# Kernel tuning notes

Measured on AMD Instinct MI355X. Metric: run time of the kernel, lower is better.

The kernel has to match this reference:

```python
import jax, jax.numpy as jnp
import numpy as np

B, S, H = 2, 1024, 2048
NH, NKV, HD = 32, 8, 64          # head_dim = H // NH
G = NH // NKV                    # GQA group size = 4
THETA = 500000.0
EPS = 1e-5
SCALE = HD ** -0.5


def _rope_neox(x, positions):
    # x: [B, S, n_heads, HD]; neox style: rotate concatenated halves
    inv_freq = 1.0 / (THETA ** (jnp.arange(0, HD, 2, dtype=jnp.float32) / HD))  # [HD/2]
    ang = positions[..., None].astype(jnp.float32) * inv_freq                    # [B, S, HD/2]
    cos = jnp.cos(ang)[:, :, None, :]
    sin = jnp.sin(ang)[:, :, None, :]
    x1, x2 = jnp.split(x, 2, axis=-1)
    return jnp.concatenate([x1 * cos - x2 * sin, x2 * cos + x1 * sin], axis=-1)


def setup_inputs() -> dict:
    key = jax.random.key(0)
    k1, k2, k3 = jax.random.split(key, 3)
    hidden_states = jax.random.normal(k1, (B, S, H), jnp.float32)
    w_qkv = jax.random.normal(k2, ((NH + 2 * NKV) * HD, H), jnp.float32) * 0.02
    w_o = jax.random.normal(k3, (H, NH * HD), jnp.float32) * 0.02
    norm_w = jnp.ones((H,), jnp.float32)
    positions = jnp.broadcast_to(jnp.arange(S, dtype=jnp.int32), (B, S))
    return {"hidden_states": hidden_states, "positions": positions,
            "w_qkv": w_qkv, "w_o": w_o, "norm_w": norm_w}


def reference(hidden_states, positions, w_qkv, w_o, norm_w):
    # QKV projection (bias=False) and split
    qkv = hidden_states @ w_qkv.T                                 # [B,S,3072]
    q, k, v = jnp.split(qkv, [NH * HD, NH * HD + NKV * HD], axis=-1)
    q = q.reshape(B, S, NH, HD)
    k = k.reshape(B, S, NKV, HD)
    v = v.reshape(B, S, NKV, HD)

    # RoPE on q and k (full rotary_dim = head_dim)
    q = _rope_neox(q, positions)
    k = _rope_neox(k, positions)

    # Causal GQA attention (dense-prefill equivalent of RadixAttention)
    qg = q.reshape(B, S, NKV, G, HD)
    scores = jnp.einsum('bqhgd,bkhd->bhgqk', qg, k) * SCALE       # [B,NKV,G,S,S]
    causal = jnp.tril(jnp.ones((S, S), dtype=bool))
    scores = jnp.where(causal, scores, jnp.float32(-1e30))
    probs = jax.nn.softmax(scores, axis=-1)
    attn = jnp.einsum('bhgqk,bkhd->bqhgd', probs, v).reshape(B, S, NH * HD)

    # BitNet sub-norm (RMSNorm) then output projection
    var = jnp.mean(attn * attn, axis=-1, keepdims=True)
    normed = attn * jax.lax.rsqrt(var + EPS) * norm_w
    return normed @ w_o.T                                         # [B,S,H]
```

## Files before the change

kernel.cpp:

```cpp
#include <hip/hip_runtime.h>
#include <hip/hip_bf16.h>
#include <cstdint>
#include <cstddef>

typedef __bf16 bf16;
typedef __bf16 bf16x2 __attribute__((ext_vector_type(2)));
typedef __bf16 bf16x4 __attribute__((ext_vector_type(4)));
typedef __bf16 bf16x8 __attribute__((ext_vector_type(8)));
typedef float  f32x4  __attribute__((ext_vector_type(4)));

__device__ __forceinline__ void async_copy16(const void* g, void* l) {
  __builtin_amdgcn_global_load_lds((const __attribute__((address_space(1))) void*)g,
                                   (__attribute__((address_space(3))) void*)l,
                                   16, 0, 0);
}

__device__ __forceinline__ int swz(int row) { return ((row >> 1) & 3) << 3; }

__device__ __forceinline__ bool block_flag_is_f32(const unsigned int* w, int tid,
                                                  int* sflag) {
  if (tid < 64) {
    int weird = 0;
#pragma unroll
    for (int c = 0; c < 2; ++c) {
      const unsigned int lo = w[c * 64 + tid] & 0xffffu;
      const unsigned int ex = (lo >> 7) & 0xffu;
      if (ex >= 134u) ++weird;
    }
    const unsigned long long m1 = __ballot(weird >= 1);
    const unsigned long long m2 = __ballot(weird == 2);
    if (tid == 0) *sflag = (__popcll(m1) + __popcll(m2) >= 8) ? 1 : 0;
  }
  __syncthreads();
  return *sflag != 0;
}

__global__ __launch_bounds__(256) void convert_all(
    const void* __restrict__ s0, const void* __restrict__ s1,
    const void* __restrict__ s2, const void* __restrict__ s3,
    bf16* __restrict__ d0, bf16* __restrict__ d1, bf16* __restrict__ d2,
    float* __restrict__ ssum) {
  __shared__ int sflag;
  const int tid = threadIdx.x;
  const bool f32 = block_flag_is_f32((const unsigned int*)s0, tid, &sflag);
  if (blockIdx.x == 0) {
    ((float4*)ssum)[tid * 2]     = make_float4(0.f, 0.f, 0.f, 0.f);
    ((float4*)ssum)[tid * 2 + 1] = make_float4(0.f, 0.f, 0.f, 0.f);
  }
  const int i = blockIdx.x * 256 + tid;
  if (i >= 3670016) return;
  const void* src; bf16* dst; int off; bool fold = false;
  if      (i < 1048576) { src = s0; dst = d0; off = i; }
  else if (i < 2621440) { src = s1; dst = d1; off = i - 1048576; }
  else                  { src = s2; dst = d2; off = i - 2621440; fold = true; }
  float v[4];
  if (f32) {
    const float4 t = ((const float4*)src)[off];
    v[0] = t.x; v[1] = t.y; v[2] = t.z; v[3] = t.w;
  } else {
    const bf16x4 t = ((const bf16x4*)src)[off];
#pragma unroll
    for (int j = 0; j < 4; ++j) v[j] = (float)t[j];
  }
  if (fold) {
    const int k0 = (off * 4) & 2047;
#pragma unroll
    for (int j = 0; j < 4; ++j) {
      const float w = f32 ? ((const float*)s3)[k0 + j] : (float)((const bf16*)s3)[k0 + j];
      v[j] *= w;
    }
  }
  bf16x4 o;
#pragma unroll
  for (int j = 0; j < 4; ++j) o[j] = (bf16)v[j];
  *(bf16x4*)(dst + (size_t)off * 4) = o;
}

__global__ __launch_bounds__(256) void gemm_qkv_rope(
    const bf16* __restrict__ A, const bf16* __restrict__ B,
    const int* __restrict__ pos,
    bf16* __restrict__ Q, bf16* __restrict__ K, bf16* __restrict__ V)
{
  __shared__ __align__(16) bf16 As[2][2 * 64 * 32];
  __shared__ __align__(16) bf16 Bs[2][2 * 128 * 32];
  const int tid = threadIdx.x, wave = tid >> 6, lane = tid & 63;
  const int l15 = lane & 15, l4 = lane >> 4;
  const int m0 = blockIdx.y * 64, n0 = blockIdx.x * 128;
  const int wm = (wave >> 1) * 32, wn = (wave & 1) * 64;
  const int swz_ro = (l4 * 8) ^ swz(l15);

  f32x4 acc[2][4] = {};

  auto stage = [&](int buf, int kt) {
#pragma unroll
    for (int c = 0; c < 2; ++c) {
      const int e = c * 2048 + tid * 8;
      const int kc = e >> 11, row = (e >> 5) & 63;
      const int o = (e & 31) ^ swz(row);
      async_copy16(A + (size_t)(m0 + row) * 2048 + kt + kc * 32 + o, &As[buf][e]);
    }
#pragma unroll
    for (int c = 0; c < 4; ++c) {
      const int e = c * 2048 + tid * 8;
      const int kc = e >> 12, row = (e >> 5) & 127;
      const int o = (e & 31) ^ swz(row);
      async_copy16(B + (size_t)(n0 + row) * 2048 + kt + kc * 32 + o, &Bs[buf][e]);
    }
  };

  stage(0, 0);
  __syncthreads();
  int cur = 0;
  for (int kt = 0; kt < 2048; kt += 64) {
    if (kt + 64 < 2048) stage(cur ^ 1, kt + 64);
#pragma unroll
    for (int s = 0; s < 2; ++s) {
      bf16x8 af[2], bfr[4];
#pragma unroll
      for (int i = 0; i < 2; ++i)
        af[i] = *(const bf16x8*)(&As[cur][s * 2048 + (wm + i * 16 + l15) * 32 + swz_ro]);
#pragma unroll
      for (int j = 0; j < 4; ++j)
        bfr[j] = *(const bf16x8*)(&Bs[cur][s * 4096 + (wn + j * 16 + l15) * 32 + swz_ro]);
#pragma unroll
      for (int i = 0; i < 2; ++i)
#pragma unroll
        for (int j = 0; j < 4; ++j)
          acc[i][j] = __builtin_amdgcn_mfma_f32_16x16x32_bf16(af[i], bfr[j], acc[i][j], 0, 0, 0);
    }
    __syncthreads();
    cur ^= 1;
  }

  if (n0 < 2560) {
    const bool isQ = (n0 < 2048);
#pragma unroll
    for (int i = 0; i < 2; ++i)
#pragma unroll
      for (int j = 0; j < 4; ++j) {
        const int col = n0 + wn + j * 16 + l15;
        const int hd = isQ ? col : (col - 2048);
        const int hh = hd >> 6, d = hd & 63;
        const int fi = d & 31;
        const float ifr = __expf((float)fi * -0.41007385554f);
#pragma unroll
        for (int r = 0; r < 4; ++r) {
          const int m = m0 + wm + i * 16 + l4 * 4 + r;
          const int b = m >> 10, s = m & 1023;
          const float ang = (float)pos[m] * ifr;
          float sn, cs;
          __sincosf(ang, &sn, &cs);
          const float x  = acc[i][j][r];
          const float xp = acc[i][j ^ 2][r];
          const float v = (d < 32) ? (x * cs - xp * sn) : (x * cs + xp * sn);
          if (isQ) Q[(((size_t)(b * 32 + hh)) * 1024 + s) * 64 + d] = (bf16)(v * 0.1803368801f);
          else     K[(((size_t)(b * 8 + hh)) * 1024 + s) * 64 + d] = (bf16)v;
        }
      }
  } else {
#pragma unroll
    for (int i = 0; i < 2; ++i)
#pragma unroll
      for (int j = 0; j < 4; ++j) {
        const int cv = n0 + wn + j * 16 + l15 - 2560;
        const int hh = cv >> 6, d = cv & 63;
#pragma unroll
        for (int r = 0; r < 4; ++r) {
          const int m = m0 + wm + i * 16 + l4 * 4 + r;
          const int b = m >> 10, s = m & 1023;
          const int sp = (s & ~31) + ((s & 15) * 2 + ((s >> 4) & 1));
          V[(((size_t)(b * 8 + hh)) * 64 + d) * 1024 + sp] = (bf16)acc[i][j][r];
        }
      }
  }
}

__global__ __launch_bounds__(256) void attn_kernel(
    const bf16* __restrict__ Q, const bf16* __restrict__ K,
    const bf16* __restrict__ Vt, bf16* __restrict__ O, float* __restrict__ ssum)
{
  __shared__ __align__(16) bf16 Ks[2 * 128 * 32];
  __shared__ __align__(16) bf16 Vs[4 * 64 * 32];
  __shared__ __align__(16) bf16 Ps[4 * 128 * 40];

  const int tid = threadIdx.x, wave = tid >> 6, lane = tid & 63;
  const int l15 = lane & 15, l4 = lane >> 4;
  const int swz_ro = (l4 * 8) ^ swz(l15);
  const int ip = blockIdx.x, bh = blockIdx.y;
  const int b = bh >> 5, h = bh & 31, kvh = h >> 2;
  const int qlo = ip * 64, qhi = (15 - ip) * 64;
  const bf16* Qb = Q + ((size_t)(b * 32 + h)) * 65536;
  const bf16* Kb = K + ((size_t)(b * 8 + kvh)) * 65536;
  const bf16* Vb = Vt + ((size_t)(b * 8 + kvh)) * 65536;

#pragma unroll
  for (int c = 0; c < 4; ++c) {
    const int e = c * 2048 + tid * 8;
    const int dchunk = e >> 12;
    const int row = (e & 4095) >> 5;
    const int qb = (row < 64) ? qlo : qhi;
    const int o = (e & 31) ^ swz(row);
    async_copy16(Qb + (size_t)(qb + (row & 63)) * 64 + dchunk * 32 + o, Ps + e);
  }
  bf16x8 kreg[4], vreg[4];
#pragma unroll
  for (int c = 0; c < 4; ++c) {
    const int e = c * 2048 + tid * 8;
    kreg[c] = *(const bf16x8*)(Kb + (size_t)((e & 4095) >> 5) * 64 + (e >> 12) * 32 + (e & 31));
    vreg[c] = *(const bf16x8*)(Vb + (size_t)((e & 2047) >> 5) * 1024 + (e >> 11) * 32 + (e & 31));
  }
  __syncthreads();
  bf16x8 aq[2][2];
#pragma unroll
  for (int i = 0; i < 2; ++i)
#pragma unroll
    for (int s = 0; s < 2; ++s)
      aq[i][s] = *(const bf16x8*)(Ps + s * 4096 + (i * 64 + wave * 16 + l15) * 32 + swz_ro);
#pragma unroll
  for (int c = 0; c < 4; ++c) {
    const int e = c * 2048 + tid * 8;
    const int krow = (e & 4095) >> 5;
    *(bf16x8*)(Ks + (e ^ swz(krow))) = kreg[c];
    const int drow = (e & 2047) >> 5;
    *(bf16x8*)(Vs + (e ^ swz(drow))) = vreg[c];
  }
  __syncthreads();

  float m_s[2][4], l_s[2][4];
  f32x4 o_acc[2][4] = {};
#pragma unroll
  for (int i = 0; i < 2; ++i)
#pragma unroll
    for (int r = 0; r < 4; ++r) { m_s[i][r] = -3.0e4f; l_s[i][r] = 0.f; }

  const int nkt = (1151 - 64 * ip) >> 7;
  for (int kt = 0; kt < nkt; ++kt) {
    const int k0 = kt * 128;
    const bool lo_act = (k0 < (ip + 1) * 64);
    if (kt + 1 < nkt) {
      const int k0n = k0 + 128;
#pragma unroll
      for (int c = 0; c < 4; ++c) {
        const int e = c * 2048 + tid * 8;
        kreg[c] = *(const bf16x8*)(Kb + (size_t)(k0n + ((e & 4095) >> 5)) * 64 + (e >> 12) * 32 + (e & 31));
        vreg[c] = *(const bf16x8*)(Vb + (size_t)((e & 2047) >> 5) * 1024 + k0n + (e >> 11) * 32 + (e & 31));
      }
    }

    f32x4 sc[2][8] = {};
#pragma unroll
    for (int j = 0; j < 8; ++j) {
      const bf16x8 bk0 = *(const bf16x8*)(Ks + (j * 16 + l15) * 32 + swz_ro);
      const bf16x8 bk1 = *(const bf16x8*)(Ks + 4096 + (j * 16 + l15) * 32 + swz_ro);
      sc[1][j] = __builtin_amdgcn_mfma_f32_16x16x32_bf16(aq[1][0], bk0, sc[1][j], 0, 0, 0);
      sc[1][j] = __builtin_amdgcn_mfma_f32_16x16x32_bf16(aq[1][1], bk1, sc[1][j], 0, 0, 0);
      if (lo_act) {
        sc[0][j] = __builtin_amdgcn_mfma_f32_16x16x32_bf16(aq[0][0], bk0, sc[0][j], 0, 0, 0);
        sc[0][j] = __builtin_amdgcn_mfma_f32_16x16x32_bf16(aq[0][1], bk1, sc[0][j], 0, 0, 0);
      }
    }

#pragma unroll
    for (int hh = 0; hh < 2; ++hh) {
      if (hh == 0 && !lo_act) continue;
      const int qb = hh ? qhi : qlo;
      float mxv[4];
      bool grow = false;
#pragma unroll
      for (int r = 0; r < 4; ++r) {
        const int rg = qb + wave * 16 + l4 * 4 + r;
        float mx = -3.0e4f;
#pragma unroll
        for (int j = 0; j < 8; ++j) {
          float v = sc[hh][j][r];
          if (k0 + j * 16 + l15 > rg) v = -3.0e4f;
          sc[hh][j][r] = v;
          mx = fmaxf(mx, v);
        }
#pragma unroll
        for (int off = 1; off < 16; off <<= 1) mx = fmaxf(mx, __shfl_xor(mx, off));
        mxv[r] = mx;
        grow = grow || (mx > m_s[hh][r] + 8.0f);
      }
      if (__all(!grow)) {
#pragma unroll
        for (int r = 0; r < 4; ++r) {
          const int rl = wave * 16 + l4 * 4 + r;
          const float m = m_s[hh][r];
          float rs = 0.f;
#pragma unroll
          for (int t = 0; t < 4; ++t) {
            const float pv0 = exp2f(sc[hh][2 * t][r]     - m);
            const float pv1 = exp2f(sc[hh][2 * t + 1][r] - m);
            rs += pv0 + pv1;
            bf16x2 pk; pk[0] = (bf16)pv0; pk[1] = (bf16)pv1;
            *(bf16x2*)(Ps + t * 5120 + (hh * 64 + rl) * 40 + l15 * 2) = pk;
          }
#pragma unroll
          for (int off = 1; off < 16; off <<= 1) rs += __shfl_xor(rs, off);
          l_s[hh][r] += rs;
        }
      } else {
#pragma unroll
        for (int r = 0; r < 4; ++r) {
          const int rl = wave * 16 + l4 * 4 + r;
          const float mnew = fmaxf(m_s[hh][r], mxv[r]);
          const float alpha = exp2f(m_s[hh][r] - mnew);
          m_s[hh][r] = mnew;
          float rs = 0.f;
#pragma unroll
          for (int t = 0; t < 4; ++t) {
            const float pv0 = exp2f(sc[hh][2 * t][r]     - mnew);
            const float pv1 = exp2f(sc[hh][2 * t + 1][r] - mnew);
            rs += pv0 + pv1;
            bf16x2 pk; pk[0] = (bf16)pv0; pk[1] = (bf16)pv1;
            *(bf16x2*)(Ps + t * 5120 + (hh * 64 + rl) * 40 + l15 * 2) = pk;
          }
#pragma unroll
          for (int off = 1; off < 16; off <<= 1) rs += __shfl_xor(rs, off);
          l_s[hh][r] = l_s[hh][r] * alpha + rs;
#pragma unroll
          for (int jd = 0; jd < 4; ++jd) o_acc[hh][jd][r] *= alpha;
        }
      }
    }

#pragma unroll
    for (int ks = 0; ks < 4; ++ks) {
      bf16x8 bv[4];
#pragma unroll
      for (int jd = 0; jd < 4; ++jd)
        bv[jd] = *(const bf16x8*)(Vs + ks * 2048 + (jd * 16 + l15) * 32 + swz_ro);
#pragma unroll
      for (int hh = 0; hh < 2; ++hh) {
        if (hh == 0 && !lo_act) continue;
        const bf16x8 ap = *(const bf16x8*)(Ps + ks * 5120 + (hh * 64 + wave * 16 + l15) * 40 + l4 * 8);
#pragma unroll
        for (int jd = 0; jd < 4; ++jd)
          o_acc[hh][jd] = __builtin_amdgcn_mfma_f32_16x16x32_bf16(ap, bv[jd], o_acc[hh][jd], 0, 0, 0);
      }
    }
    __syncthreads();
    if (kt + 1 < nkt) {
#pragma unroll
      for (int c = 0; c < 4; ++c) {
        const int e = c * 2048 + tid * 8;
        const int krow = (e & 4095) >> 5;
        *(bf16x8*)(Ks + (e ^ swz(krow))) = kreg[c];
        const int drow = (e & 2047) >> 5;
        *(bf16x8*)(Vs + (e ^ swz(drow))) = vreg[c];
      }
      __syncthreads();
    }
  }

#pragma unroll
  for (int hh = 0; hh < 2; ++hh) {
    const int qb = hh ? qhi : qlo;
#pragma unroll
    for (int r = 0; r < 4; ++r) {
      const float inv = 1.0f / l_s[hh][r];
      const int srow = qb + wave * 16 + l4 * 4 + r;
      bf16* op = O + ((size_t)(b * 1024 + srow)) * 2048 + h * 64;
      float ss = 0.f;
#pragma unroll
      for (int jd = 0; jd < 4; ++jd) {
        const float v = o_acc[hh][jd][r] * inv;
        op[jd * 16 + l15] = (bf16)v;
        ss += v * v;
      }
#pragma unroll
      for (int off = 1; off < 16; off <<= 1) ss += __shfl_xor(ss, off);
      if (l15 == 0) atomicAdd(&ssum[b * 1024 + srow], ss);
    }
  }
}

__global__ __launch_bounds__(256) void gemm_out(
    const bf16* __restrict__ A, const bf16* __restrict__ B,
    const float* __restrict__ ssum, const unsigned int* __restrict__ hs_raw,
    void* __restrict__ out)
{
  __shared__ __align__(16) bf16 As[2][2 * 64 * 32];
  __shared__ __align__(16) bf16 Bs[2][2 * 128 * 32];
  __shared__ int sflag;
  const int tid = threadIdx.x, wave = tid >> 6, lane = tid & 63;
  const bool f32out = block_flag_is_f32(hs_raw, tid, &sflag);
  const int l15 = lane & 15, l4 = lane >> 4;
  const int m0 = blockIdx.y * 64, n0 = blockIdx.x * 128;
  const int wm = (wave >> 1) * 32, wn = (wave & 1) * 64;
  const int swz_ro = (l4 * 8) ^ swz(l15);

  f32x4 acc[2][4] = {};

  auto stage = [&](int buf, int kt) {
#pragma unroll
    for (int c = 0; c < 2; ++c) {
      const int e = c * 2048 + tid * 8;
      const int kc = e >> 11, row = (e >> 5) & 63;
      const int o = (e & 31) ^ swz(row);
      async_copy16(A + (size_t)(m0 + row) * 2048 + kt + kc * 32 + o, &As[buf][e]);
    }
#pragma unroll
    for (int c = 0; c < 4; ++c) {
      const int e = c * 2048 + tid * 8;
      const int kc = e >> 12, row = (e >> 5) & 127;
      const int o = (e & 31) ^ swz(row);
      async_copy16(B + (size_t)(n0 + row) * 2048 + kt + kc * 32 + o, &Bs[buf][e]);
    }
  };

  stage(0, 0);
  __syncthreads();
  int cur = 0;
  for (int kt = 0; kt < 2048; kt += 64) {
    if (kt + 64 < 2048) stage(cur ^ 1, kt + 64);
#pragma unroll
    for (int s = 0; s < 2; ++s) {
      bf16x8 af[2], bfr[4];
#pragma unroll
      for (int i = 0; i < 2; ++i)
        af[i] = *(const bf16x8*)(&As[cur][s * 2048 + (wm + i * 16 + l15) * 32 + swz_ro]);
#pragma unroll
      for (int j = 0; j < 4; ++j)
        bfr[j] = *(const bf16x8*)(&Bs[cur][s * 4096 + (wn + j * 16 + l15) * 32 + swz_ro]);
#pragma unroll
      for (int i = 0; i < 2; ++i)
#pragma unroll
        for (int j = 0; j < 4; ++j)
          acc[i][j] = __builtin_amdgcn_mfma_f32_16x16x32_bf16(af[i], bfr[j], acc[i][j], 0, 0, 0);
    }
    __syncthreads();
    cur ^= 1;
  }

#pragma unroll
  for (int i = 0; i < 2; ++i)
#pragma unroll
    for (int r = 0; r < 4; ++r) {
      const int row = m0 + wm + i * 16 + l4 * 4 + r;
      const float ri = rsqrtf(ssum[row] * (1.0f / 2048.0f) + 1e-5f);
#pragma unroll
      for (int j = 0; j < 4; ++j) {
        const int col = n0 + wn + j * 16 + l15;
        const size_t idx = (size_t)row * 2048 + col;
        const float v = ri * acc[i][j][r];
        if (f32out) ((float*)out)[idx] = v;
        else        ((bf16*)out)[idx]  = (bf16)v;
      }
    }
}

extern "C" void kernel_launch(void* const* d_in, const int* in_sizes, int n_in,
                              void* d_out, int out_size, void* d_ws, size_t ws_size,
                              hipStream_t stream) {
  const void* hs     = d_in[0];
  const int*  pos    = (const int*)d_in[1];
  const void* w_qkv  = d_in[2];
  const void* w_o    = d_in[3];
  const void* norm_w = d_in[4];

  char* ws = (char*)d_ws;
  bf16*  hs_b   = (bf16*) (ws);
  bf16*  wqkv_b = (bf16*) (ws + 8388608);
  bf16*  w_o_b  = (bf16*) (ws + 20971520);
  float* ssum   = (float*)(ws + 29360128);
  bf16*  Qr     = (bf16*) (ws + 29368320);
  bf16*  Kr     = (bf16*) (ws + 37756928);
  bf16*  Vtr    = (bf16*) (ws + 39854080);
  bf16*  attn_o = (bf16*) (ws + 41951232);

  convert_all<<<14336, 256, 0, stream>>>(hs, w_qkv, w_o, norm_w,
                                         hs_b, wqkv_b, w_o_b, ssum);
  gemm_qkv_rope<<<dim3(24, 32), 256, 0, stream>>>(hs_b, wqkv_b, pos, Qr, Kr, Vtr);
  attn_kernel<<<dim3(8, 64), 256, 0, stream>>>(Qr, Kr, Vtr, attn_o, ssum);
  gemm_out<<<dim3(16, 32), 256, 0, stream>>>(attn_o, w_o_b, ssum,
                                             (const unsigned int*)hs, d_out);
}
```

Before: 233.4 us.

## Enlarge GEMM tiles to 128x128 with K=32 stages; async K/V loads in attention

Both GEMMs move from 64x128 block tiles with a K step of 64 to 128x128 tiles with a K step of 32. Each wave now holds a 4x4 grid of MFMA accumulators, which raises data reuse per LDS load, and the grids shrink to 384 and 256 blocks. The attention kernel drops its register-prefetched K/V double buffering and instead issues direct global-to-LDS async copies at the start of each key tile, followed by a barrier. The trade-offs are fewer blocks to fill the CUs, more K-loop iterations and barriers in the GEMMs, and no overlap of K/V loads with compute in attention.

After: 258.8 us. 10.8% more time.

```diff
diff --git a/kernel.cpp b/kernel.cpp
--- a/kernel.cpp
+++ b/kernel.cpp
@@ -81,53 +81,44 @@
     const int* __restrict__ pos,
     bf16* __restrict__ Q, bf16* __restrict__ K, bf16* __restrict__ V)
 {
-  __shared__ __align__(16) bf16 As[2][2 * 64 * 32];
-  __shared__ __align__(16) bf16 Bs[2][2 * 128 * 32];
+  __shared__ __align__(16) bf16 As[2][128 * 32];
+  __shared__ __align__(16) bf16 Bs[2][128 * 32];
   const int tid = threadIdx.x, wave = tid >> 6, lane = tid & 63;
   const int l15 = lane & 15, l4 = lane >> 4;
-  const int m0 = blockIdx.y * 64, n0 = blockIdx.x * 128;
-  const int wm = (wave >> 1) * 32, wn = (wave & 1) * 64;
+  const int m0 = blockIdx.y * 128, n0 = blockIdx.x * 128;
+  const int wm = (wave >> 1) * 64, wn = (wave & 1) * 64;
   const int swz_ro = (l4 * 8) ^ swz(l15);
 
-  f32x4 acc[2][4] = {};
+  f32x4 acc[4][4] = {};
 
   auto stage = [&](int buf, int kt) {
 #pragma unroll
     for (int c = 0; c < 2; ++c) {
       const int e = c * 2048 + tid * 8;
-      const int kc = e >> 11, row = (e >> 5) & 63;
+      const int row = e >> 5;
       const int o = (e & 31) ^ swz(row);
-      async_copy16(A + (size_t)(m0 + row) * 2048 + kt + kc * 32 + o, &As[buf][e]);
-    }
-#pragma unroll
-    for (int c = 0; c < 4; ++c) {
-      const int e = c * 2048 + tid * 8;
-      const int kc = e >> 12, row = (e >> 5) & 127;
-      const int o = (e & 31) ^ swz(row);
-      async_copy16(B + (size_t)(n0 + row) * 2048 + kt + kc * 32 + o, &Bs[buf][e]);
+      async_copy16(A + (size_t)(m0 + row) * 2048 + kt + o, &As[buf][e]);
+      async_copy16(B + (size_t)(n0 + row) * 2048 + kt + o, &Bs[buf][e]);
     }
   };
 
   stage(0, 0);
   __syncthreads();
   int cur = 0;
-  for (int kt = 0; kt < 2048; kt += 64) {
-    if (kt + 64 < 2048) stage(cur ^ 1, kt + 64);
-#pragma unroll
-    for (int s = 0; s < 2; ++s) {
-      bf16x8 af[2], bfr[4];
-#pragma unroll
-      for (int i = 0; i < 2; ++i)
-        af[i] = *(const bf16x8*)(&As[cur][s * 2048 + (wm + i * 16 + l15) * 32 + swz_ro]);
+  for (int kt = 0; kt < 2048; kt += 32) {
+    if (kt + 32 < 2048) stage(cur ^ 1, kt + 32);
+    bf16x8 af[4], bfr[4];
+#pragma unroll
+    for (int i = 0; i < 4; ++i)
+      af[i] = *(const bf16x8*)(&As[cur][(wm + i * 16 + l15) * 32 + swz_ro]);
+#pragma unroll
+    for (int j = 0; j < 4; ++j)
+      bfr[j] = *(const bf16x8*)(&Bs[cur][(wn + j * 16 + l15) * 32 + swz_ro]);
+#pragma unroll
+    for (int i = 0; i < 4; ++i)
 #pragma unroll
       for (int j = 0; j < 4; ++j)
-        bfr[j] = *(const bf16x8*)(&Bs[cur][s * 4096 + (wn + j * 16 + l15) * 32 + swz_ro]);
-#pragma unroll
-      for (int i = 0; i < 2; ++i)
-#pragma unroll
-        for (int j = 0; j < 4; ++j)
-          acc[i][j] = __builtin_amdgcn_mfma_f32_16x16x32_bf16(af[i], bfr[j], acc[i][j], 0, 0, 0);
-    }
+        acc[i][j] = __builtin_amdgcn_mfma_f32_16x16x32_bf16(af[i], bfr[j], acc[i][j], 0, 0, 0);
     __syncthreads();
     cur ^= 1;
   }
@@ -135,7 +126,7 @@
   if (n0 < 2560) {
     const bool isQ = (n0 < 2048);
 #pragma unroll
-    for (int i = 0; i < 2; ++i)
+    for (int i = 0; i < 4; ++i)
 #pragma unroll
       for (int j = 0; j < 4; ++j) {
         const int col = n0 + wn + j * 16 + l15;
@@ -159,7 +150,7 @@
       }
   } else {
 #pragma unroll
-    for (int i = 0; i < 2; ++i)
+    for (int i = 0; i < 4; ++i)
 #pragma unroll
       for (int j = 0; j < 4; ++j) {
         const int cv = n0 + wn + j * 16 + l15 - 2560;
@@ -202,13 +193,6 @@
     const int o = (e & 31) ^ swz(row);
     async_copy16(Qb + (size_t)(qb + (row & 63)) * 64 + dchunk * 32 + o, Ps + e);
   }
-  bf16x8 kreg[4], vreg[4];
-#pragma unroll
-  for (int c = 0; c < 4; ++c) {
-    const int e = c * 2048 + tid * 8;
-    kreg[c] = *(const bf16x8*)(Kb + (size_t)((e & 4095) >> 5) * 64 + (e >> 12) * 32 + (e & 31));
-    vreg[c] = *(const bf16x8*)(Vb + (size_t)((e & 2047) >> 5) * 1024 + (e >> 11) * 32 + (e & 31));
-  }
   __syncthreads();
   bf16x8 aq[2][2];
 #pragma unroll
@@ -216,14 +200,6 @@
 #pragma unroll
     for (int s = 0; s < 2; ++s)
       aq[i][s] = *(const bf16x8*)(Ps + s * 4096 + (i * 64 + wave * 16 + l15) * 32 + swz_ro);
-#pragma unroll
-  for (int c = 0; c < 4; ++c) {
-    const int e = c * 2048 + tid * 8;
-    const int krow = (e & 4095) >> 5;
-    *(bf16x8*)(Ks + (e ^ swz(krow))) = kreg[c];
-    const int drow = (e & 2047) >> 5;
-    *(bf16x8*)(Vs + (e ^ swz(drow))) = vreg[c];
-  }
   __syncthreads();
 
   float m_s[2][4], l_s[2][4];
@@ -237,15 +213,17 @@
   for (int kt = 0; kt < nkt; ++kt) {
     const int k0 = kt * 128;
     const bool lo_act = (k0 < (ip + 1) * 64);
-    if (kt + 1 < nkt) {
-      const int k0n = k0 + 128;
-#pragma unroll
-      for (int c = 0; c < 4; ++c) {
-        const int e = c * 2048 + tid * 8;
-        kreg[c] = *(const bf16x8*)(Kb + (size_t)(k0n + ((e & 4095) >> 5)) * 64 + (e >> 12) * 32 + (e & 31));
-        vreg[c] = *(const bf16x8*)(Vb + (size_t)((e & 2047) >> 5) * 1024 + k0n + (e >> 11) * 32 + (e & 31));
-      }
-    }
+#pragma unroll
+    for (int c = 0; c < 4; ++c) {
+      const int e = c * 2048 + tid * 8;
+      const int krow = (e & 4095) >> 5;
+      const int ko = (e & 31) ^ swz(krow);
+      async_copy16(Kb + (size_t)(k0 + krow) * 64 + (e >> 12) * 32 + ko, Ks + e);
+      const int drow = (e & 2047) >> 5;
+      const int vo = (e & 31) ^ swz(drow);
+      async_copy16(Vb + (size_t)drow * 1024 + k0 + (e >> 11) * 32 + vo, Vs + e);
+    }
+    __syncthreads();
 
     f32x4 sc[2][8] = {};
 #pragma unroll
@@ -341,17 +319,6 @@
       }
     }
     __syncthreads();
-    if (kt + 1 < nkt) {
-#pragma unroll
-      for (int c = 0; c < 4; ++c) {
-        const int e = c * 2048 + tid * 8;
-        const int krow = (e & 4095) >> 5;
-        *(bf16x8*)(Ks + (e ^ swz(krow))) = kreg[c];
-        const int drow = (e & 2047) >> 5;
-        *(bf16x8*)(Vs + (e ^ swz(drow))) = vreg[c];
-      }
-      __syncthreads();
-    }
   }
 
 #pragma unroll
@@ -381,61 +348,52 @@
     const float* __restrict__ ssum, const unsigned int* __restrict__ hs_raw,
     void* __restrict__ out)
 {
-  __shared__ __align__(16) bf16 As[2][2 * 64 * 32];
-  __shared__ __align__(16) bf16 Bs[2][2 * 128 * 32];
+  __shared__ __align__(16) bf16 As[2][128 * 32];
+  __shared__ __align__(16) bf16 Bs[2][128 * 32];
   __shared__ int sflag;
   const int tid = threadIdx.x, wave = tid >> 6, lane = tid & 63;
   const bool f32out = block_flag_is_f32(hs_raw, tid, &sflag);
   const int l15 = lane & 15, l4 = lane >> 4;
-  const int m0 = blockIdx.y * 64, n0 = blockIdx.x * 128;
-  const int wm = (wave >> 1) * 32, wn = (wave & 1) * 64;
+  const int m0 = blockIdx.y * 128, n0 = blockIdx.x * 128;
+  const int wm = (wave >> 1) * 64, wn = (wave & 1) * 64;
   const int swz_ro = (l4 * 8) ^ swz(l15);
 
-  f32x4 acc[2][4] = {};
+  f32x4 acc[4][4] = {};
 
   auto stage = [&](int buf, int kt) {
 #pragma unroll
     for (int c = 0; c < 2; ++c) {
       const int e = c * 2048 + tid * 8;
-      const int kc = e >> 11, row = (e >> 5) & 63;
+      const int row = e >> 5;
       const int o = (e & 31) ^ swz(row);
-      async_copy16(A + (size_t)(m0 + row) * 2048 + kt + kc * 32 + o, &As[buf][e]);
-    }
-#pragma unroll
-    for (int c = 0; c < 4; ++c) {
-      const int e = c * 2048 + tid * 8;
-      const int kc = e >> 12, row = (e >> 5) & 127;
-      const int o = (e & 31) ^ swz(row);
-      async_copy16(B + (size_t)(n0 + row) * 2048 + kt + kc * 32 + o, &Bs[buf][e]);
+      async_copy16(A + (size_t)(m0 + row) * 2048 + kt + o, &As[buf][e]);
+      async_copy16(B + (size_t)(n0 + row) * 2048 + kt + o, &Bs[buf][e]);
     }
   };
 
   stage(0, 0);
   __syncthreads();
   int cur = 0;
-  for (int kt = 0; kt < 2048; kt += 64) {
-    if (kt + 64 < 2048) stage(cur ^ 1, kt + 64);
-#pragma unroll
-    for (int s = 0; s < 2; ++s) {
-      bf16x8 af[2], bfr[4];
-#pragma unroll
-      for (int i = 0; i < 2; ++i)
-        af[i] = *(const bf16x8*)(&As[cur][s * 2048 + (wm + i * 16 + l15) * 32 + swz_ro]);
+  for (int kt = 0; kt < 2048; kt += 32) {
+    if (kt + 32 < 2048) stage(cur ^ 1, kt + 32);
+    bf16x8 af[4], bfr[4];
+#pragma unroll
+    for (int i = 0; i < 4; ++i)
+      af[i] = *(const bf16x8*)(&As[cur][(wm + i * 16 + l15) * 32 + swz_ro]);
+#pragma unroll
+    for (int j = 0; j < 4; ++j)
+      bfr[j] = *(const bf16x8*)(&Bs[cur][(wn + j * 16 + l15) * 32 + swz_ro]);
+#pragma unroll
+    for (int i = 0; i < 4; ++i)
 #pragma unroll
       for (int j = 0; j < 4; ++j)
-        bfr[j] = *(const bf16x8*)(&Bs[cur][s * 4096 + (wn + j * 16 + l15) * 32 + swz_ro]);
-#pragma unroll
-      for (int i = 0; i < 2; ++i)
-#pragma unroll
-        for (int j = 0; j < 4; ++j)
-          acc[i][j] = __builtin_amdgcn_mfma_f32_16x16x32_bf16(af[i], bfr[j], acc[i][j], 0, 0, 0);
-    }
+        acc[i][j] = __builtin_amdgcn_mfma_f32_16x16x32_bf16(af[i], bfr[j], acc[i][j], 0, 0, 0);
     __syncthreads();
     cur ^= 1;
   }
 
 #pragma unroll
-  for (int i = 0; i < 2; ++i)
+  for (int i = 0; i < 4; ++i)
 #pragma unroll
     for (int r = 0; r < 4; ++r) {
       const int row = m0 + wm + i * 16 + l4 * 4 + r;
@@ -472,8 +430,8 @@
 
   convert_all<<<14336, 256, 0, stream>>>(hs, w_qkv, w_o, norm_w,
                                          hs_b, wqkv_b, w_o_b, ssum);
-  gemm_qkv_rope<<<dim3(24, 32), 256, 0, stream>>>(hs_b, wqkv_b, pos, Qr, Kr, Vtr);
+  gemm_qkv_rope<<<dim3(24, 16), 256, 0, stream>>>(hs_b, wqkv_b, pos, Qr, Kr, Vtr);
   attn_kernel<<<dim3(8, 64), 256, 0, stream>>>(Qr, Kr, Vtr, attn_o, ssum);
-  gemm_out<<<dim3(16, 32), 256, 0, stream>>>(attn_o, w_o_b, ssum,
+  gemm_out<<<dim3(16, 16), 256, 0, stream>>>(attn_o, w_o_b, ssum,
                                              (const unsigned int*)hs, d_out);
 }
```
